# Kernel optimization log

Measured on AMD Instinct MI355X. Metric: run time of the kernel, lower is better.

## Reference

```python
import jax, jax.numpy as jnp
import numpy as np

IN_F = 512
OUT_F = 512
NOISE_DIM = 128
BATCH = 512
OUT_DIM = IN_F * OUT_F + OUT_F  # 262656
PRIOR_STD = 1.0
PRIOR_SCALE = 1.0
POSTERIOR_SCALE = 1.0


def setup_inputs() -> dict:
    key = jax.random.key(0)
    k1, k2, k3, k4, k5, k6 = jax.random.split(key, 6)
    x = jax.random.normal(k1, (BATCH, IN_F), dtype=jnp.float32)
    prior_x = jax.random.normal(k2, (BATCH, IN_F), dtype=jnp.float32)
    hyper_noise = jax.random.normal(k3, (BATCH, NOISE_DIM), dtype=jnp.float32)
    # hypermodel = nn.Linear(noise_dim, out_dim): kaiming-uniform-ish init approximated by uniform
    bound = 1.0 / np.sqrt(NOISE_DIM)
    hW = jax.random.uniform(k4, (OUT_DIM, NOISE_DIM), jnp.float32, -bound, bound)
    hb = jax.random.uniform(k5, (OUT_DIM,), jnp.float32, -bound, bound)
    # PriorHyperLinear: row-normalized gaussian weight scaled by prior_std (eye), zero bias (prior_mean=0)
    pW = jax.random.normal(k6, (OUT_DIM, NOISE_DIM), dtype=jnp.float32)
    pW = PRIOR_STD * pW / jnp.linalg.norm(pW, axis=1, keepdims=True)
    pb = jnp.zeros((OUT_DIM,), dtype=jnp.float32)
    return {"x": x, "prior_x": prior_x, "hyper_noise": hyper_noise,
            "hW": hW, "hb": hb, "pW": pW, "pb": pb}


def _base_forward(x, params):
    # params: [B, in*out + out] -> per-sample weight [B, in, out], bias [B, out]
    weight = params[:, : IN_F * OUT_F].reshape(-1, IN_F, OUT_F)
    bias = params[:, IN_F * OUT_F:]  # [B, out]
    # bmm(x[:,None,:], weight) + bias -> [B, out]
    return jnp.einsum("bi,bio->bo", x, weight) + bias


def reference(x, prior_x, hyper_noise, hW, hb, pW, pb):
    params = hyper_noise @ hW.T + hb  # [B, out_dim]
    out = _base_forward(x, params)
    prior_params = hyper_noise @ pW.T + pb
    prior_out = _base_forward(prior_x, prior_params)
    return out * POSTERIOR_SCALE + prior_out * PRIOR_SCALE
```

## Files before the change

kernel.cpp:

```cpp
#include <hip/hip_runtime.h>
#include <hip/hip_fp16.h>

#define BATCH 512
#define INF   512
#define OUTF  512
#define ND    128
#define WPART 262144

typedef __attribute__((ext_vector_type(8))) _Float16 half8;
typedef __attribute__((ext_vector_type(2))) _Float16 half2v;
typedef __attribute__((ext_vector_type(4))) float    f32x4;

__device__ inline half8 cvt8(float4 a, float4 b) {
  half2v h0 = __builtin_bit_cast(half2v, __builtin_amdgcn_cvt_pkrtz(a.x, a.y));
  half2v h1 = __builtin_bit_cast(half2v, __builtin_amdgcn_cvt_pkrtz(a.z, a.w));
  half2v h2 = __builtin_bit_cast(half2v, __builtin_amdgcn_cvt_pkrtz(b.x, b.y));
  half2v h3 = __builtin_bit_cast(half2v, __builtin_amdgcn_cvt_pkrtz(b.z, b.w));
  half8 r = { h0[0], h0[1], h1[0], h1[1], h2[0], h2[1], h3[0], h3[1] };
  return r;
}

__global__ void __launch_bounds__(256) transpose_kernel(
    const float* __restrict__ x, const float* __restrict__ px,
    float* __restrict__ xt) {
  __shared__ float t[32][33];
  const float* src = blockIdx.z ? px : x;
  float* dst = xt + ((size_t)blockIdx.z << 18);
  const int bi = blockIdx.x * 32, bb = blockIdx.y * 32;
  const int tx = threadIdx.x & 31, ty = threadIdx.x >> 5;
  #pragma unroll
  for (int r = 0; r < 32; r += 8)
    t[ty + r][tx] = src[(size_t)(bb + ty + r) * 512 + bi + tx];
  __syncthreads();
  #pragma unroll
  for (int r = 0; r < 32; r += 8)
    dst[(size_t)(bi + ty + r) * 512 + bb + tx] = t[tx][ty + r];
}

__global__ void __launch_bounds__(256) tail_kernel(
    const float* __restrict__ hn, const float* __restrict__ hW,
    const float* __restrict__ pW, float* __restrict__ TT) {
  const int bt = blockIdx.x & 7;
  const int bg = blockIdx.x >> 3;
  __shared__ float wsum[64][132];
  __shared__ float hs[32][132];
  {
    int r = threadIdx.x >> 2, seg = threadIdx.x & 3;
    const float4* h4 = (const float4*)(hW + (((size_t)(WPART + bt*64 + r)) << 7) + seg*32);
    const float4* p4 = (const float4*)(pW + (((size_t)(WPART + bt*64 + r)) << 7) + seg*32);
    #pragma unroll
    for (int qq = 0; qq < 8; ++qq) {
      float4 a = h4[qq], b = p4[qq];
      float* d = &wsum[r][seg*32 + qq*4];
      d[0]=a.x+b.x; d[1]=a.y+b.y; d[2]=a.z+b.z; d[3]=a.w+b.w;
    }
    int bb = threadIdx.x >> 3, ch = threadIdx.x & 7;
    const float4* hh = (const float4*)(hn + (((size_t)(bg*32 + bb)) << 7) + ch*16);
    #pragma unroll
    for (int qq = 0; qq < 4; ++qq) {
      float4 a = hh[qq];
      float* d = &hs[bb][ch*16 + qq*4];
      d[0]=a.x; d[1]=a.y; d[2]=a.z; d[3]=a.w;
    }
  }
  __syncthreads();
  const int ol = threadIdx.x & 63, b0 = (threadIdx.x >> 6) * 8;
  float a[8] = {};
  for (int n = 0; n < 128; n += 4) {
    float4 wv = *(const float4*)&wsum[ol][n];
    #pragma unroll
    for (int r = 0; r < 8; ++r) {
      float4 hv = *(const float4*)&hs[b0 + r][n];
      a[r] += hv.x*wv.x + hv.y*wv.y + hv.z*wv.z + hv.w*wv.w;
    }
  }
  #pragma unroll
  for (int r = 0; r < 8; ++r)
    TT[(((size_t)(bg*32 + b0 + r)) << 9) + bt*64 + ol] = a[r];
}

__global__ void __launch_bounds__(1024, 4) gemm_kernel(
    const float* __restrict__ xt, const float* __restrict__ hn,
    const float* __restrict__ hW, const float* __restrict__ pW,
    float* __restrict__ P, int S) {
  const int tid = threadIdx.x;
  const int lane = tid & 63, w = tid >> 6;
  const int l15 = lane & 15, j = lane >> 4;
  const int wrow0 = w << 5;

  const int n0 = blockIdx.x << 6;
  const int q  = blockIdx.y;
  const int spb  = S >> 3;
  const int half = S >> 1;
  const int part = q / half;
  const int rem  = q % half;
  const int nh   = rem / spb;
  const int irange = 512 / spb;
  const int i0   = (rem % spb) * irange;
  const int nst  = irange >> 1;
  const float* srcW = part ? pW : hW;
  const float* xtp  = xt + ((size_t)part << 18);
  const int woff = nh << 5;

  __shared__ half8 ldsW[2][512];
  __shared__ float xr[2][2][512];

  f32x4 acc[2][4] = {};

  const int o_s = tid >> 4;
  const int g_s = tid & 15;
  const int isub_s = g_s >> 3;
  const size_t colbase = (((size_t)(n0 + o_s)) << 7) + woff + ((g_s & 7) << 2);
  const int wdst = (o_s << 7) + (((((g_s >> 1)) ^ (o_s & 7)) << 4) | ((g_s & 1) << 3));

  half8 hnf[2];
  #pragma unroll
  for (int m = 0; m < 2; ++m) {
    int row = wrow0 + m * 16 + l15;
    const float4* hp = (const float4*)(hn + ((size_t)row << 7) + woff + (j << 3));
    hnf[m] = cvt8(hp[0], hp[1]);
  }

  auto loadW = [&](int ph, float4& rw) {
    int i = i0 + 2 * ph + isub_s;
    rw = *(const float4*)(srcW + ((size_t)i << 16) + colbase);
  };
  auto writeW = [&](int buf, float4 rw) {
    unsigned u0 = __builtin_bit_cast(unsigned, __builtin_amdgcn_cvt_pkrtz(rw.x, rw.y));
    unsigned u1 = __builtin_bit_cast(unsigned, __builtin_amdgcn_cvt_pkrtz(rw.z, rw.w));
    uint2 u; u.x = u0; u.y = u1;
    *(uint2*)((char*)&ldsW[buf][0] + wdst) = u;
  };
  auto stageX = [&](int buf, int ph) {
    int i = i0 + 2 * ph + (tid >> 9);
    const float* g = xtp + ((size_t)i << 9) + (tid & 511);
    __builtin_amdgcn_global_load_lds(
        (const __attribute__((address_space(1))) void*)g,
        (__attribute__((address_space(3))) void*)((char*)&xr[buf][0][0] + tid * 4),
        4, 0, 0);
  };
  auto compute = [&](int buf) {
    const char* bW = (const char*)&ldsW[buf][0];
    #pragma unroll
    for (int kk = 0; kk < 2; ++kk) {
      half8 af[2], bf[4];
      #pragma unroll
      for (int m = 0; m < 2; ++m) {
        float xv = xr[buf][kk][wrow0 + m * 16 + l15];
        _Float16 t = (_Float16)xv;
        half8 xb = { t, t, t, t, t, t, t, t };
        af[m] = hnf[m] * xb;
      }
      #pragma unroll
      for (int nn = 0; nn < 4; ++nn) {
        int byte = (((nn << 4) + l15) << 7) + (((((kk << 2) + j)) ^ (l15 & 7)) << 4);
        bf[nn] = *(const half8*)(bW + byte);
      }
      __builtin_amdgcn_s_setprio(1);
      #pragma unroll
      for (int m = 0; m < 2; ++m)
        #pragma unroll
        for (int nn = 0; nn < 4; ++nn)
          acc[m][nn] = __builtin_amdgcn_mfma_f32_16x16x32_f16(
              af[m], bf[nn], acc[m][nn], 0, 0, 0);
      __builtin_amdgcn_s_setprio(0);
    }
  };

  float4 rwA, rwB;
  asm volatile("s_waitcnt vmcnt(0)" ::: "memory");
  loadW(0, rwA);
  stageX(0, 0);
  loadW(1, rwB);
  writeW(0, rwA);

  for (int p = 0; p < nst; p += 2) {
    asm volatile("s_waitcnt vmcnt(1) lgkmcnt(0)" ::: "memory");
    __builtin_amdgcn_s_barrier();
    stageX(1, p + 1);
    if (p + 2 < nst) loadW(p + 2, rwA);
    compute(0);
    writeW(1, rwB);

    if (p + 2 < nst)
      asm volatile("s_waitcnt vmcnt(1) lgkmcnt(0)" ::: "memory");
    else
      asm volatile("s_waitcnt vmcnt(0) lgkmcnt(0)" ::: "memory");
    __builtin_amdgcn_s_barrier();
    if (p + 2 < nst) stageX(0, p + 2);
    if (p + 3 < nst) loadW(p + 3, rwB);
    compute(1);
    if (p + 2 < nst) writeW(0, rwA);
  }

  float* outp = P + ((size_t)q << 18);
  #pragma unroll
  for (int m = 0; m < 2; ++m) {
    int row = wrow0 + m * 16 + (j << 2);
    #pragma unroll
    for (int nn = 0; nn < 4; ++nn) {
      int col = n0 + (nn << 4) + l15;
      float* op = outp + (size_t)row * OUTF + col;
      op[0]    = acc[m][nn][0];
      op[512]  = acc[m][nn][1];
      op[1024] = acc[m][nn][2];
      op[1536] = acc[m][nn][3];
    }
  }
}

__global__ void __launch_bounds__(256) finish_kernel(
    const float* __restrict__ P, const float* __restrict__ x,
    const float* __restrict__ hb, const float* __restrict__ TT,
    float* __restrict__ out, int S) {
  const int o  = blockIdx.x * 256 + threadIdx.x;
  const int b0 = blockIdx.y * 4;
  __shared__ float xs[4][512];
  #pragma unroll
  for (int t = 0; t < 8; ++t) {
    int idx = threadIdx.x + t * 256;
    xs[idx >> 9][idx & 511] = x[((size_t)(b0 + (idx >> 9)) << 9) + (idx & 511)];
  }
  __syncthreads();

  const float bias = hb[WPART + o];
  float a0 = bias, a1 = bias, a2 = bias, a3 = bias;
  #pragma unroll 8
  for (int i = 0; i < 512; ++i) {
    float hv = hb[(i << 9) + o];
    a0 += xs[0][i] * hv; a1 += xs[1][i] * hv;
    a2 += xs[2][i] * hv; a3 += xs[3][i] * hv;
  }
  a0 += TT[((size_t)b0 << 9) + o];
  a1 += TT[((size_t)(b0 + 1) << 9) + o];
  a2 += TT[((size_t)(b0 + 2) << 9) + o];
  a3 += TT[((size_t)(b0 + 3) << 9) + o];

  const float* Pp = P + ((size_t)b0 << 9) + o;
  float t0 = 0, t1 = 0, t2 = 0, t3 = 0;
  for (int k = 0; k < S; ++k) {
    const float* qq = Pp + ((size_t)k << 18);
    t0 += qq[0]; t1 += qq[512]; t2 += qq[1024]; t3 += qq[1536];
  }
  out[((size_t)b0 << 9) + o]       = a0 + t0;
  out[((size_t)(b0 + 1) << 9) + o] = a1 + t1;
  out[((size_t)(b0 + 2) << 9) + o] = a2 + t2;
  out[((size_t)(b0 + 3) << 9) + o] = a3 + t3;
}

extern "C" void kernel_launch(void* const* d_in, const int* in_sizes, int n_in,
                              void* d_out, int out_size, void* d_ws, size_t ws_size,
                              hipStream_t stream) {
  const float* x  = (const float*)d_in[0];
  const float* px = (const float*)d_in[1];
  const float* hn = (const float*)d_in[2];
  const float* hW = (const float*)d_in[3];
  const float* hb = (const float*)d_in[4];
  const float* pW = (const float*)d_in[5];
  float* out = (float*)d_out;
  float* xt  = (float*)d_ws;
  float* TT  = xt + (1 << 19);
  float* P   = TT + (1 << 18);

  int S = 32;
  while (S > 8 && (((size_t)(3 + S)) << 20) > ws_size) S >>= 1;

  transpose_kernel<<<dim3(16, 16, 2), 256, 0, stream>>>(x, px, xt);
  tail_kernel<<<dim3(128), 256, 0, stream>>>(hn, hW, pW, TT);
  gemm_kernel<<<dim3(8, S), dim3(1024), 0, stream>>>(xt, hn, hW, pW, P, S);
  finish_kernel<<<dim3(2, 128), dim3(256), 0, stream>>>(P, x, hb, TT, out, S);
}
```

Baseline: 134.3 us.

## Restructure hypernetwork GEMM: per-block i-slab with all noise bands, drop transpose

```diff
diff --git a/kernel.cpp b/kernel.cpp
--- a/kernel.cpp
+++ b/kernel.cpp
@@ -6,6 +6,7 @@
 #define OUTF  512
 #define ND    128
 #define WPART 262144
+#define NSLOT 32
 
 typedef __attribute__((ext_vector_type(8))) _Float16 half8;
 typedef __attribute__((ext_vector_type(2))) _Float16 half2v;
@@ -18,23 +19,6 @@
   half2v h3 = __builtin_bit_cast(half2v, __builtin_amdgcn_cvt_pkrtz(b.z, b.w));
   half8 r = { h0[0], h0[1], h1[0], h1[1], h2[0], h2[1], h3[0], h3[1] };
   return r;
-}
-
-__global__ void __launch_bounds__(256) transpose_kernel(
-    const float* __restrict__ x, const float* __restrict__ px,
-    float* __restrict__ xt) {
-  __shared__ float t[32][33];
-  const float* src = blockIdx.z ? px : x;
-  float* dst = xt + ((size_t)blockIdx.z << 18);
-  const int bi = blockIdx.x * 32, bb = blockIdx.y * 32;
-  const int tx = threadIdx.x & 31, ty = threadIdx.x >> 5;
-  #pragma unroll
-  for (int r = 0; r < 32; r += 8)
-    t[ty + r][tx] = src[(size_t)(bb + ty + r) * 512 + bi + tx];
-  __syncthreads();
-  #pragma unroll
-  for (int r = 0; r < 32; r += 8)
-    dst[(size_t)(bi + ty + r) * 512 + bb + tx] = t[tx][ty + r];
 }
 
 __global__ void __launch_bounds__(256) tail_kernel(
@@ -79,173 +63,182 @@
     TT[(((size_t)(bg*32 + b0 + r)) << 9) + bt*64 + ol] = a[r];
 }
 
-__global__ void __launch_bounds__(1024, 4) gemm_kernel(
-    const float* __restrict__ xt, const float* __restrict__ hn,
-    const float* __restrict__ hW, const float* __restrict__ pW,
-    float* __restrict__ P, int S) {
+__global__ void __launch_bounds__(512, 4) gemm_kernel(
+    const float* __restrict__ x, const float* __restrict__ px,
+    const float* __restrict__ hn, const float* __restrict__ hW,
+    const float* __restrict__ pW, float* __restrict__ P) {
   const int tid = threadIdx.x;
   const int lane = tid & 63, w = tid >> 6;
   const int l15 = lane & 15, j = lane >> 4;
-  const int wrow0 = w << 5;
-
-  const int n0 = blockIdx.x << 6;
-  const int q  = blockIdx.y;
-  const int spb  = S >> 3;
-  const int half = S >> 1;
-  const int part = q / half;
-  const int rem  = q % half;
-  const int nh   = rem / spb;
-  const int irange = 512 / spb;
-  const int i0   = (rem % spb) * irange;
-  const int nst  = irange >> 1;
+  const int wm = w >> 1, wn = w & 1;
+
+  const int q  = blockIdx.x;
+  const int nt = blockIdx.y;
+  const int n0 = nt << 5;
+  const int part   = q >> 4;
+  const int i0     = (q & 15) << 5;
   const float* srcW = part ? pW : hW;
-  const float* xtp  = xt + ((size_t)part << 18);
-  const int woff = nh << 5;
-
-  __shared__ half8 ldsW[2][512];
-  __shared__ float xr[2][2][512];
-
-  f32x4 acc[2][4] = {};
+  const float* srcX = part ? px : x;
+
+  __shared__ half8 ldsW[2][256];
+  __shared__ unsigned short xh[512][32];
+
+  f32x4 acc[8] = {};
+
+  {
+    const int rsub = tid >> 3, ch = tid & 7;
+    const int g = ch >> 1, sub = ch & 1;
+    #pragma unroll
+    for (int r = 0; r < 8; ++r) {
+      int row = r * 64 + rsub;
+      float4 v = *(const float4*)(srcX + ((size_t)row << 9) + i0 + ch * 4);
+      unsigned u0 = __builtin_bit_cast(unsigned, __builtin_amdgcn_cvt_pkrtz(v.x, v.y));
+      unsigned u1 = __builtin_bit_cast(unsigned, __builtin_amdgcn_cvt_pkrtz(v.z, v.w));
+      uint2 uu; uu.x = u0; uu.y = u1;
+      *(uint2*)((char*)xh + row * 64 + ((g ^ (row & 3)) << 4) + sub * 8) = uu;
+    }
+  }
 
   const int o_s = tid >> 4;
-  const int g_s = tid & 15;
-  const int isub_s = g_s >> 3;
-  const size_t colbase = (((size_t)(n0 + o_s)) << 7) + woff + ((g_s & 7) << 2);
-  const int wdst = (o_s << 7) + (((((g_s >> 1)) ^ (o_s & 7)) << 4) | ((g_s & 1) << 3));
-
-  half8 hnf[2];
-  #pragma unroll
-  for (int m = 0; m < 2; ++m) {
-    int row = wrow0 + m * 16 + l15;
-    const float4* hp = (const float4*)(hn + ((size_t)row << 7) + woff + (j << 3));
-    hnf[m] = cvt8(hp[0], hp[1]);
-  }
-
-  auto loadW = [&](int ph, float4& rw) {
-    int i = i0 + 2 * ph + isub_s;
-    rw = *(const float4*)(srcW + ((size_t)i << 16) + colbase);
-  };
-  auto writeW = [&](int buf, float4 rw) {
-    unsigned u0 = __builtin_bit_cast(unsigned, __builtin_amdgcn_cvt_pkrtz(rw.x, rw.y));
-    unsigned u1 = __builtin_bit_cast(unsigned, __builtin_amdgcn_cvt_pkrtz(rw.z, rw.w));
-    uint2 u; u.x = u0; u.y = u1;
-    *(uint2*)((char*)&ldsW[buf][0] + wdst) = u;
-  };
-  auto stageX = [&](int buf, int ph) {
-    int i = i0 + 2 * ph + (tid >> 9);
-    const float* g = xtp + ((size_t)i << 9) + (tid & 511);
-    __builtin_amdgcn_global_load_lds(
-        (const __attribute__((address_space(1))) void*)g,
-        (__attribute__((address_space(3))) void*)((char*)&xr[buf][0][0] + tid * 4),
-        4, 0, 0);
-  };
-  auto compute = [&](int buf) {
-    const char* bW = (const char*)&ldsW[buf][0];
-    #pragma unroll
-    for (int kk = 0; kk < 2; ++kk) {
-      half8 af[2], bf[4];
+  const int seg = tid & 15;
+  const int isub_s = seg >> 3;
+  const int nl_s   = (seg & 7) << 2;
+  const int wg     = (isub_s << 2) + ((seg & 7) >> 1);
+  const int wbyte  = (o_s << 7) + (((wg ^ (o_s & 7))) << 4) + ((seg & 1) << 3);
+
+  for (int band = 0; band < 4; ++band) {
+    const int woff = band << 5;
+
+    half8 hnf[8];
+    #pragma unroll
+    for (int m = 0; m < 8; ++m) {
+      int row = wm * 128 + m * 16 + l15;
+      const float4* hp = (const float4*)(hn + ((size_t)row << 7) + woff + (j << 3));
+      hnf[m] = cvt8(hp[0], hp[1]);
+    }
+
+    auto loadW = [&](int ph, float4& rw) {
+      int i = i0 + 2 * ph + isub_s;
+      rw = *(const float4*)(srcW +
+          (((size_t)((i << 9) + n0 + o_s)) << 7) + woff + nl_s);
+    };
+    auto writeW = [&](int buf, float4 rw) {
+      unsigned u0 = __builtin_bit_cast(unsigned, __builtin_amdgcn_cvt_pkrtz(rw.x, rw.y));
+      unsigned u1 = __builtin_bit_cast(unsigned, __builtin_amdgcn_cvt_pkrtz(rw.z, rw.w));
+      uint2 uu; uu.x = u0; uu.y = u1;
+      *(uint2*)((char*)ldsW + buf * 4096 + wbyte) = uu;
+    };
+    auto compute = [&](int buf, int p) {
+      const char* WB = (const char*)ldsW + buf * 4096;
+      half8 bf0, bf1;
+      {
+        int col = wn * 16 + l15;
+        int cb  = col << 7;
+        bf0 = *(const half8*)(WB + cb + (((j     ) ^ (col & 7)) << 4));
+        bf1 = *(const half8*)(WB + cb + (((4 + j) ^ (col & 7)) << 4));
+      }
+      half2v hx[8];
       #pragma unroll
-      for (int m = 0; m < 2; ++m) {
-        float xv = xr[buf][kk][wrow0 + m * 16 + l15];
-        _Float16 t = (_Float16)xv;
-        half8 xb = { t, t, t, t, t, t, t, t };
-        af[m] = hnf[m] * xb;
-      }
-      #pragma unroll
-      for (int nn = 0; nn < 4; ++nn) {
-        int byte = (((nn << 4) + l15) << 7) + (((((kk << 2) + j)) ^ (l15 & 7)) << 4);
-        bf[nn] = *(const half8*)(bW + byte);
+      for (int m = 0; m < 8; ++m) {
+        int row = wm * 128 + m * 16 + l15;
+        unsigned xw = *(const unsigned*)((const char*)xh + row * 64 +
+            ((((p >> 2)) ^ (row & 3)) << 4) + ((4 * p) & 15));
+        hx[m] = __builtin_bit_cast(half2v, xw);
       }
       __builtin_amdgcn_s_setprio(1);
       #pragma unroll
-      for (int m = 0; m < 2; ++m)
-        #pragma unroll
-        for (int nn = 0; nn < 4; ++nn)
-          acc[m][nn] = __builtin_amdgcn_mfma_f32_16x16x32_f16(
-              af[m], bf[nn], acc[m][nn], 0, 0, 0);
+      for (int m = 0; m < 8; ++m) {
+        _Float16 lo = hx[m][0];
+        half8 xb = { lo, lo, lo, lo, lo, lo, lo, lo };
+        acc[m] = __builtin_amdgcn_mfma_f32_16x16x32_f16(hnf[m] * xb, bf0, acc[m], 0, 0, 0);
+      }
+      #pragma unroll
+      for (int m = 0; m < 8; ++m) {
+        _Float16 hi = hx[m][1];
+        half8 xb = { hi, hi, hi, hi, hi, hi, hi, hi };
+        acc[m] = __builtin_amdgcn_mfma_f32_16x16x32_f16(hnf[m] * xb, bf1, acc[m], 0, 0, 0);
+      }
       __builtin_amdgcn_s_setprio(0);
-    }
-  };
-
-  float4 rwA, rwB;
-  asm volatile("s_waitcnt vmcnt(0)" ::: "memory");
-  loadW(0, rwA);
-  stageX(0, 0);
-  loadW(1, rwB);
-  writeW(0, rwA);
-
-  for (int p = 0; p < nst; p += 2) {
-    asm volatile("s_waitcnt vmcnt(1) lgkmcnt(0)" ::: "memory");
+    };
+
+    float4 rwA, rwB;
+    loadW(0, rwA);
+    loadW(1, rwB);
+    writeW(0, rwA);
+    asm volatile("s_waitcnt lgkmcnt(0)" ::: "memory");
     __builtin_amdgcn_s_barrier();
-    stageX(1, p + 1);
-    if (p + 2 < nst) loadW(p + 2, rwA);
-    compute(0);
+
+    for (int p = 0; p < 14; p += 2) {
+      loadW(p + 2, rwA);
+      compute(0, p);
+      writeW(1, rwB);
+      asm volatile("s_waitcnt lgkmcnt(0)" ::: "memory");
+      __builtin_amdgcn_s_barrier();
+
+      loadW(p + 3, rwB);
+      compute(1, p + 1);
+      writeW(0, rwA);
+      asm volatile("s_waitcnt lgkmcnt(0)" ::: "memory");
+      __builtin_amdgcn_s_barrier();
+    }
+    compute(0, 14);
     writeW(1, rwB);
-
-    if (p + 2 < nst)
-      asm volatile("s_waitcnt vmcnt(1) lgkmcnt(0)" ::: "memory");
-    else
-      asm volatile("s_waitcnt vmcnt(0) lgkmcnt(0)" ::: "memory");
+    asm volatile("s_waitcnt lgkmcnt(0)" ::: "memory");
     __builtin_amdgcn_s_barrier();
-    if (p + 2 < nst) stageX(0, p + 2);
-    if (p + 3 < nst) loadW(p + 3, rwB);
-    compute(1);
-    if (p + 2 < nst) writeW(0, rwA);
+    compute(1, 15);
+    __builtin_amdgcn_s_barrier();
   }
 
   float* outp = P + ((size_t)q << 18);
   #pragma unroll
-  for (int m = 0; m < 2; ++m) {
-    int row = wrow0 + m * 16 + (j << 2);
-    #pragma unroll
-    for (int nn = 0; nn < 4; ++nn) {
-      int col = n0 + (nn << 4) + l15;
-      float* op = outp + (size_t)row * OUTF + col;
-      op[0]    = acc[m][nn][0];
-      op[512]  = acc[m][nn][1];
-      op[1024] = acc[m][nn][2];
-      op[1536] = acc[m][nn][3];
-    }
+  for (int m = 0; m < 8; ++m) {
+    int row = wm * 128 + m * 16 + (j << 2);
+    int col = n0 + wn * 16 + l15;
+    float* op = outp + (size_t)row * OUTF + col;
+    op[0]    = acc[m][0];
+    op[512]  = acc[m][1];
+    op[1024] = acc[m][2];
+    op[1536] = acc[m][3];
   }
 }
 
 __global__ void __launch_bounds__(256) finish_kernel(
     const float* __restrict__ P, const float* __restrict__ x,
     const float* __restrict__ hb, const float* __restrict__ TT,
-    float* __restrict__ out, int S) {
+    float* __restrict__ out) {
   const int o  = blockIdx.x * 256 + threadIdx.x;
-  const int b0 = blockIdx.y * 4;
-  __shared__ float xs[4][512];
+  const int b0 = blockIdx.y * 2;
+  __shared__ float xs[2][512];
   #pragma unroll
-  for (int t = 0; t < 8; ++t) {
+  for (int t = 0; t < 4; ++t) {
     int idx = threadIdx.x + t * 256;
     xs[idx >> 9][idx & 511] = x[((size_t)(b0 + (idx >> 9)) << 9) + (idx & 511)];
   }
   __syncthreads();
 
   const float bias = hb[WPART + o];
-  float a0 = bias, a1 = bias, a2 = bias, a3 = bias;
-  #pragma unroll 8
+  float a0 = bias, a1 = bias;
+  #pragma unroll 16
   for (int i = 0; i < 512; ++i) {
     float hv = hb[(i << 9) + o];
-    a0 += xs[0][i] * hv; a1 += xs[1][i] * hv;
-    a2 += xs[2][i] * hv; a3 += xs[3][i] * hv;
+    a0 += xs[0][i] * hv;
+    a1 += xs[1][i] * hv;
   }
   a0 += TT[((size_t)b0 << 9) + o];
   a1 += TT[((size_t)(b0 + 1) << 9) + o];
-  a2 += TT[((size_t)(b0 + 2) << 9) + o];
-  a3 += TT[((size_t)(b0 + 3) << 9) + o];
-
-  const float* Pp = P + ((size_t)b0 << 9) + o;
-  float t0 = 0, t1 = 0, t2 = 0, t3 = 0;
-  for (int k = 0; k < S; ++k) {
-    const float* qq = Pp + ((size_t)k << 18);
-    t0 += qq[0]; t1 += qq[512]; t2 += qq[1024]; t3 += qq[1536];
-  }
-  out[((size_t)b0 << 9) + o]       = a0 + t0;
-  out[((size_t)(b0 + 1) << 9) + o] = a1 + t1;
-  out[((size_t)(b0 + 2) << 9) + o] = a2 + t2;
-  out[((size_t)(b0 + 3) << 9) + o] = a3 + t3;
+
+  const float* P0 = P + ((size_t)b0 << 9) + o;
+  const float* P1 = P0 + 512;
+  float t00 = 0, t01 = 0, t10 = 0, t11 = 0;
+  #pragma unroll 4
+  for (int k = 0; k < NSLOT; k += 2) {
+    t00 += P0[(size_t)(k)     << 18];
+    t01 += P0[(size_t)(k + 1) << 18];
+    t10 += P1[(size_t)(k)     << 18];
+    t11 += P1[(size_t)(k + 1) << 18];
+  }
+  out[((size_t)b0 << 9) + o]       = a0 + t00 + t01;
+  out[((size_t)(b0 + 1) << 9) + o] = a1 + t10 + t11;
 }
 
 extern "C" void kernel_launch(void* const* d_in, const int* in_sizes, int n_in,
@@ -258,15 +251,10 @@
   const float* hb = (const float*)d_in[4];
   const float* pW = (const float*)d_in[5];
   float* out = (float*)d_out;
-  float* xt  = (float*)d_ws;
-  float* TT  = xt + (1 << 19);
+  float* TT  = (float*)d_ws;
   float* P   = TT + (1 << 18);
 
-  int S = 32;
-  while (S > 8 && (((size_t)(3 + S)) << 20) > ws_size) S >>= 1;
-
-  transpose_kernel<<<dim3(16, 16, 2), 256, 0, stream>>>(x, px, xt);
   tail_kernel<<<dim3(128), 256, 0, stream>>>(hn, hW, pW, TT);
-  gemm_kernel<<<dim3(8, S), dim3(1024), 0, stream>>>(xt, hn, hW, pW, P, S);
-  finish_kernel<<<dim3(2, 128), dim3(256), 0, stream>>>(P, x, hb, TT, out, S);
-}
+  gemm_kernel<<<dim3(NSLOT, 16), dim3(512), 0, stream>>>(x, px, hn, hW, pW, P);
+  finish_kernel<<<dim3(2, 256), dim3(256), 0, stream>>>(P, x, hb, TT, out);
+}
```

New measurement: 133.6 us. About the same (-0.5%).
